# Performance work log

Measured on AMD Instinct MI355X. Metric: run time of the kernel, lower is better.

## Reference

```python
import jax, jax.numpy as jnp
import numpy as np

ALPHA = 0.5
BETA = 5.0
LOGIT_SCALE = 100.0  # exp(log(100)) -- CLIP's learned logit scale at its clamp value
NUM_CLASSES = 200


def _l2norm(x):
    return x / jnp.linalg.norm(x, axis=-1, keepdims=True)


def setup_inputs() -> dict:
    key = jax.random.key(0)
    k1, k2, k3, k4 = jax.random.split(key, 4)
    img_f = jax.random.normal(k1, (1024, 512), dtype=jnp.float32)
    text_features = jax.random.normal(k2, (200, 512), dtype=jnp.float32)
    keys = jax.random.normal(k3, (50000, 512), dtype=jnp.float32)
    labels = jax.random.randint(k4, (50000,), 0, NUM_CLASSES, dtype=jnp.int64)
    return {"img_f": img_f, "text_features": text_features, "keys": keys, "labels": labels}


def reference(img_f, text_features, keys, labels):
    # encode_image output is L2-normalized in the module; keys were built from
    # normalized image features, text_features are normalized class embeddings.
    q = _l2norm(img_f)            # [B, D]
    t = _l2norm(text_features)    # [C, D]
    k = _l2norm(keys)             # [N, D]

    # CLIP zero-shot branch: scale * q @ t.T -> [B, C]
    z = LOGIT_SCALE * jnp.einsum('bd,cd->bc', q, t)

    # Tip-Adapter cache branch: exp(beta * q @ keys.T) @ one_hot(labels)
    sim = jnp.einsum('bd,nd->bn', q, k)                 # [B, N]
    aff = jnp.exp(BETA * sim)                           # [B, N]
    values = jax.nn.one_hot(labels, NUM_CLASSES, dtype=aff.dtype)  # [N, C]
    c = aff @ values                                    # [B, C]

    return (1.0 - ALPHA) * z + ALPHA * c
```

## Files before the change

### kernel.cpp

```cpp
#include <hip/hip_runtime.h>

#define B_Q    1024
#define D_K    512
#define N_CLS  200
#define N_KEYS 50000
#define N_PAD  50176
#define N_ZT   196
#define NT_TOT 197
#define KN_ROWS 50200
#define HS     16

#define PR0 N_KEYS
#define PR1 (PR0 + B_Q)
#define PR2 (PR1 + N_CLS)
#define PR3 (PR2 + 400)

typedef __attribute__((ext_vector_type(8))) short bf16x8;
typedef __attribute__((ext_vector_type(4))) float f32x4;

__device__ __forceinline__ unsigned short f2bf(float f) {
  union { float f; unsigned int i; } v; v.f = f;
  unsigned int r = v.i + 0x7fffu + ((v.i >> 16) & 1u);
  return (unsigned short)(r >> 16);
}
__device__ __forceinline__ uint4 pack8(const float f[8], float s) {
  uint4 o;
  o.x = (unsigned)f2bf(f[0]*s) | ((unsigned)f2bf(f[1]*s) << 16);
  o.y = (unsigned)f2bf(f[2]*s) | ((unsigned)f2bf(f[3]*s) << 16);
  o.z = (unsigned)f2bf(f[4]*s) | ((unsigned)f2bf(f[5]*s) << 16);
  o.w = (unsigned)f2bf(f[6]*s) | ((unsigned)f2bf(f[7]*s) << 16);
  return o;
}
__device__ __forceinline__ void async_copy16(const void* g, void* lds) {
  __builtin_amdgcn_global_load_lds(
      (const __attribute__((address_space(1))) unsigned int*)g,
      (__attribute__((address_space(3))) unsigned int*)lds, 16, 0, 0);
}

__global__ void k_zero(int* __restrict__ g) {
  int i = blockIdx.x * 1024 + threadIdx.x;
  if (i < 2 * N_CLS * HS) g[i] = 0;
}

__global__ __launch_bounds__(1024) void k_rank(const int* __restrict__ labels,
                                               const int* __restrict__ ghist,
                                               int* __restrict__ gcnt,
                                               int* __restrict__ perm,
                                               int* __restrict__ cls) {
  __shared__ int incl[N_CLS];
  __shared__ int histl[N_CLS];
  __shared__ int lhist[N_CLS];
  __shared__ int lbase[N_CLS];
  __shared__ int lcur[N_CLS];
  int t = threadIdx.x;
  if (t < N_CLS) {
    int h = ghist[t * HS];
    histl[t] = h; incl[t] = h; lhist[t] = 0;
  }
  __syncthreads();
  for (int d = 1; d < N_CLS; d <<= 1) {
    int x = 0;
    if (t < N_CLS && t >= d) x = incl[t - d];
    __syncthreads();
    if (t < N_CLS) incl[t] += x;
    __syncthreads();
  }
  int n = blockIdx.x * 1024 + t;
  int lab = -1;
  if (n < N_KEYS) {
    lab = labels[n];
    atomicAdd(&lhist[lab], 1);
  }
  __syncthreads();
  if (t < N_CLS && lhist[t] > 0) {
    lbase[t] = (incl[t] - histl[t]) + atomicAdd(&gcnt[t * HS], lhist[t]);
    lcur[t] = 0;
  }
  __syncthreads();
  if (n < N_KEYS) {
    int r = atomicAdd(&lcur[lab], 1);
    int d = lbase[lab] + r;
    perm[d] = n;
    cls[d] = lab;
  } else if (n < N_PAD) {
    perm[n] = N_KEYS;
    cls[n] = N_CLS;
  }
}

__global__ void k_prep2(const float* __restrict__ keys, const float* __restrict__ img,
                        const float* __restrict__ txt, const int* __restrict__ labels,
                        unsigned short* __restrict__ qn, unsigned short* __restrict__ kn,
                        int* __restrict__ ghist, float* __restrict__ out) {
  int w = threadIdx.x >> 6, lane = threadIdx.x & 63;
  int row = blockIdx.x * 4 + w;
  const float* src; unsigned short* dst;
  if (row < PR0) {
    if (lane == 0) atomicAdd(&ghist[labels[row] * HS], 1);
    src = keys + (size_t)row * D_K;
    dst = kn + (size_t)row * D_K;
  } else if (row < PR1) {
    int r = row - PR0;
    src = img + (size_t)r * D_K;
    dst = qn + (size_t)r * D_K;
  } else if (row < PR2) {
    int r = row - PR1;
    src = txt + (size_t)r * D_K;
    dst = kn + (size_t)(N_KEYS + r) * D_K;
  } else if (row < PR3) {
    int zr = row - PR2;
    uint4* o4 = (uint4*)(out + (size_t)zr * 512) + lane * 2;
    o4[0] = make_uint4(0, 0, 0, 0);
    o4[1] = make_uint4(0, 0, 0, 0);
    return;
  } else return;
  const float4* s4 = (const float4*)src + lane * 2;
  float4 a = s4[0], b = s4[1];
  float f[8] = {a.x, a.y, a.z, a.w, b.x, b.y, b.z, b.w};
  float ss = 0.f;
#pragma unroll
  for (int i = 0; i < 8; i++) ss += f[i] * f[i];
#pragma unroll
  for (int d = 1; d < 64; d <<= 1) ss += __shfl_xor(ss, d);
  float rinv = rsqrtf(ss);
  *((uint4*)dst + lane) = pack8(f, rinv);
}

__global__ __launch_bounds__(512, 2) void k_main(const unsigned short* __restrict__ qn,
                                                 const unsigned short* __restrict__ kn,
                                                 const int* __restrict__ cls,
                                                 const int* __restrict__ perm,
                                                 float* __restrict__ out) {
  extern __shared__ unsigned short smem[];
  int t = threadIdx.x;
  int bid = blockIdx.x;
  int xcd = bid & 7, bk = bid >> 3;
  int wsw = (xcd < 4 ? xcd * 99 : 396 + (xcd - 4) * 98) + bk;
  int tileN = wsw >> 2, tileB = wsw & 3;
  int rowB0 = tileB * 256, rowN0 = tileN * 256;

  f32x4 acc[8][4];
#pragma unroll
  for (int i = 0; i < 8; i++)
#pragma unroll
    for (int j = 0; j < 4; j++) acc[i][j] = (f32x4){0.f, 0.f, 0.f, 0.f};

  int lane = t & 63, w = t >> 6;
  int wm = (w >> 2) * 128;
  int wcN = (w & 3) * 64;
  int l15 = lane & 15, lq = lane >> 4;
  const int rA = t >> 3;
  const int gsw = ((t & 7) ^ (rA & 7)) * 8;
  const int sw = l15 & 7;

  int prow[4];
  int cj[4] = {N_CLS, N_CLS, N_CLS, N_CLS};
  int cseg0 = N_CLS, cseg1 = N_CLS;
  if (tileN < N_ZT) {
#pragma unroll
    for (int c = 0; c < 4; c++) prow[c] = perm[rowN0 + c * 64 + rA];
#pragma unroll
    for (int j = 0; j < 4; j++) cj[j] = cls[rowN0 + wcN + 16 * j + l15];
    cseg0 = cls[rowN0 + wcN];
    cseg1 = cls[rowN0 + wcN + 63];
  } else {
#pragma unroll
    for (int c = 0; c < 4; c++) {
      int r = c * 64 + rA;
      prow[c] = N_KEYS + (r < N_CLS ? r : N_CLS - 1);
    }
  }

  auto stageA = [&](int p, int k0) {
    unsigned short* dst = smem + p * 16384;
#pragma unroll
    for (int c = 0; c < 4; c++)
      async_copy16(qn + (size_t)(rowB0 + c * 64 + rA) * D_K + k0 + gsw,
                   dst + c * 4096 + t * 8);
  };
  auto stageB = [&](int p, int k0) {
    unsigned short* dst = smem + 32768 + p * 16384;
#pragma unroll
    for (int c = 0; c < 4; c++)
      async_copy16(kn + (size_t)prow[c] * D_K + k0 + gsw,
                   dst + c * 4096 + t * 8);
  };
  auto quad = [&](int p, int ih, int jh) {
    const unsigned short* A = smem + p * 16384;
    const unsigned short* B = smem + 32768 + p * 16384;
    __builtin_amdgcn_s_setprio(1);
#pragma unroll
    for (int s = 0; s < 2; s++) {
      int cg = ((s * 4 + lq) ^ sw) * 8;
      bf16x8 af[4], bf[2];
#pragma unroll
      for (int i = 0; i < 4; i++) {
        int ra = wm + ih * 64 + 16 * i + l15;
        af[i] = *(const bf16x8*)&A[ra * 64 + cg];
      }
#pragma unroll
      for (int jj = 0; jj < 2; jj++) {
        int rb = wcN + (jh * 2 + jj) * 16 + l15;
        bf[jj] = *(const bf16x8*)&B[rb * 64 + cg];
      }
#pragma unroll
      for (int i = 0; i < 4; i++)
#pragma unroll
        for (int jj = 0; jj < 2; jj++)
          acc[ih * 4 + i][jh * 2 + jj] = __builtin_amdgcn_mfma_f32_16x16x32_bf16(
              af[i], bf[jj], acc[ih * 4 + i][jh * 2 + jj], 0, 0, 0);
    }
    __builtin_amdgcn_s_setprio(0);
  };

  stageA(0, 0); stageB(0, 0);
  __syncthreads();
  for (int kt = 0; kt < 8; ++kt) {
    int p = kt & 1, k0n = (kt + 1) * 64;
    if (kt < 7) stageA(p ^ 1, k0n);
    quad(p, 0, 0);
    __builtin_amdgcn_s_barrier();
    if (kt < 7) stageB(p ^ 1, k0n);
    quad(p, 0, 1);
    __builtin_amdgcn_s_barrier();
    quad(p, 1, 0);
    __builtin_amdgcn_s_barrier();
    quad(p, 1, 1);
    __syncthreads();
  }

  if (tileN >= N_ZT) {
#pragma unroll
    for (int i = 0; i < 8; i++)
#pragma unroll
      for (int j = 0; j < 4; j++) {
        int col = wcN + 16 * j + l15;
        if (col < N_CLS) {
#pragma unroll
          for (int r = 0; r < 4; r++) {
            int row = rowB0 + wm + 16 * i + lq * 4 + r;
            atomicAdd(out + (size_t)row * N_CLS + col, 50.0f * acc[i][j][r]);
          }
        }
      }
    return;
  }

#pragma unroll
  for (int i = 0; i < 8; i++)
#pragma unroll
    for (int j = 0; j < 4; j++)
#pragma unroll
      for (int r = 0; r < 4; r++) acc[i][j][r] = __expf(5.0f * acc[i][j][r]);

  for (int c = cseg0; c <= cseg1; c++) {
    if (c >= N_CLS) break;
#pragma unroll
    for (int i = 0; i < 8; i++) {
      float s0 = 0.f, s1 = 0.f, s2 = 0.f, s3 = 0.f;
#pragma unroll
      for (int j = 0; j < 4; j++) {
        if (cj[j] == c) {
          s0 += acc[i][j][0]; s1 += acc[i][j][1];
          s2 += acc[i][j][2]; s3 += acc[i][j][3];
        }
      }
#pragma unroll
      for (int d = 1; d < 16; d <<= 1) {
        s0 += __shfl_xor(s0, d); s1 += __shfl_xor(s1, d);
        s2 += __shfl_xor(s2, d); s3 += __shfl_xor(s3, d);
      }
      if (l15 == 0) {
        int row = rowB0 + wm + 16 * i + lq * 4;
        float* o = out + (size_t)row * N_CLS + c;
        if (s0 != 0.f) atomicAdd(o + 0 * N_CLS, 0.5f * s0);
        if (s1 != 0.f) atomicAdd(o + 1 * N_CLS, 0.5f * s1);
        if (s2 != 0.f) atomicAdd(o + 2 * N_CLS, 0.5f * s2);
        if (s3 != 0.f) atomicAdd(o + 3 * N_CLS, 0.5f * s3);
      }
    }
  }
}

extern "C" void kernel_launch(void* const* d_in, const int* in_sizes, int n_in,
                              void* d_out, int out_size, void* d_ws, size_t ws_size,
                              hipStream_t stream) {
  (void)in_sizes; (void)n_in; (void)out_size; (void)ws_size;
  const float* img    = (const float*)d_in[0];
  const float* txt    = (const float*)d_in[1];
  const float* keys   = (const float*)d_in[2];
  const int*   labels = (const int*)d_in[3];
  float*       out    = (float*)d_out;

  char* ws = (char*)d_ws;
  unsigned short* qn = (unsigned short*)(ws + 0);
  unsigned short* kn = (unsigned short*)(ws + 1048576);
  int*  perm = (int*)(ws + 52453376);
  int*  cls  = (int*)(ws + 52654080);
  int*  gz   = (int*)(ws + 52854784);

  hipFuncSetAttribute((const void*)k_main,
                      hipFuncAttributeMaxDynamicSharedMemorySize, 131072);

  k_zero<<<7, 1024, 0, stream>>>(gz);
  k_prep2<<<(PR3 + 3) / 4, 256, 0, stream>>>(keys, img, txt, labels, qn, kn, gz, out);
  k_rank<<<N_PAD / 1024, 1024, 0, stream>>>(labels, gz, gz + N_CLS * HS, perm, cls);
  k_main<<<dim3(4 * NT_TOT), 512, 131072, stream>>>(qn, kn, cls, perm, out);
}
```

Before: 290.1 us.

## Halve B-tile to 128 rows, doubling grid and cutting LDS and accumulators

Shrinks each block's query tile from 256 to 128 rows, so the grid doubles to 8x197 blocks, per-wave accumulators halve, and dynamic LDS drops from 128KB to 96KB. The A fragments are loaded once per k-substep and reused across both B column halves. The block-to-XCD mapping is also simplified. The aim is more blocks in flight and lower register pressure, at the cost of loading the key tiles twice as often and issuing more atomics for the class reduction.

```diff
diff --git a/kernel.cpp b/kernel.cpp
--- a/kernel.cpp
+++ b/kernel.cpp
@@ -134,20 +134,19 @@
   extern __shared__ unsigned short smem[];
   int t = threadIdx.x;
   int bid = blockIdx.x;
-  int xcd = bid & 7, bk = bid >> 3;
-  int wsw = (xcd < 4 ? xcd * 99 : 396 + (xcd - 4) * 98) + bk;
-  int tileN = wsw >> 2, tileB = wsw & 3;
-  int rowB0 = tileB * 256, rowN0 = tileN * 256;
-
-  f32x4 acc[8][4];
-#pragma unroll
-  for (int i = 0; i < 8; i++)
+  int wsw = (bid & 7) * NT_TOT + (bid >> 3);
+  int tileN = wsw >> 3, tileB = wsw & 7;
+  int rowB0 = tileB * 128, rowN0 = tileN * 256;
+
+  f32x4 acc[4][4];
+#pragma unroll
+  for (int i = 0; i < 4; i++)
 #pragma unroll
     for (int j = 0; j < 4; j++) acc[i][j] = (f32x4){0.f, 0.f, 0.f, 0.f};
 
   int lane = t & 63, w = t >> 6;
-  int wm = (w >> 2) * 128;
-  int wcN = (w & 3) * 64;
+  int wr = (w >> 2) * 64;
+  int wc = (w & 3) * 64;
   int l15 = lane & 15, lq = lane >> 4;
   const int rA = t >> 3;
   const int gsw = ((t & 7) ^ (rA & 7)) * 8;
@@ -160,9 +159,9 @@
 #pragma unroll
     for (int c = 0; c < 4; c++) prow[c] = perm[rowN0 + c * 64 + rA];
 #pragma unroll
-    for (int j = 0; j < 4; j++) cj[j] = cls[rowN0 + wcN + 16 * j + l15];
-    cseg0 = cls[rowN0 + wcN];
-    cseg1 = cls[rowN0 + wcN + 63];
+    for (int j = 0; j < 4; j++) cj[j] = cls[rowN0 + wc + 16 * j + l15];
+    cseg0 = cls[rowN0 + wc];
+    cseg1 = cls[rowN0 + wc + 63];
   } else {
 #pragma unroll
     for (int c = 0; c < 4; c++) {
@@ -172,44 +171,46 @@
   }
 
   auto stageA = [&](int p, int k0) {
-    unsigned short* dst = smem + p * 16384;
-#pragma unroll
-    for (int c = 0; c < 4; c++)
+    unsigned short* dst = smem + p * 8192;
+#pragma unroll
+    for (int c = 0; c < 2; c++)
       async_copy16(qn + (size_t)(rowB0 + c * 64 + rA) * D_K + k0 + gsw,
                    dst + c * 4096 + t * 8);
   };
   auto stageB = [&](int p, int k0) {
-    unsigned short* dst = smem + 32768 + p * 16384;
+    unsigned short* dst = smem + 16384 + p * 16384;
 #pragma unroll
     for (int c = 0; c < 4; c++)
       async_copy16(kn + (size_t)prow[c] * D_K + k0 + gsw,
                    dst + c * 4096 + t * 8);
   };
-  auto quad = [&](int p, int ih, int jh) {
-    const unsigned short* A = smem + p * 16384;
-    const unsigned short* B = smem + 32768 + p * 16384;
+
+  bf16x8 af[4];
+  auto ldA = [&](int p, int s) {
+    const unsigned short* A = smem + p * 8192;
+    int cg = ((s * 4 + lq) ^ sw) * 8;
+#pragma unroll
+    for (int i = 0; i < 4; i++) {
+      int ra = wr + 16 * i + l15;
+      af[i] = *(const bf16x8*)&A[ra * 64 + cg];
+    }
+  };
+  auto mfma8 = [&](int p, int s, int jh) {
+    const unsigned short* B = smem + 16384 + p * 16384;
+    int cg = ((s * 4 + lq) ^ sw) * 8;
+    bf16x8 bf[2];
+#pragma unroll
+    for (int jj = 0; jj < 2; jj++) {
+      int rb = wc + (jh * 2 + jj) * 16 + l15;
+      bf[jj] = *(const bf16x8*)&B[rb * 64 + cg];
+    }
     __builtin_amdgcn_s_setprio(1);
 #pragma unroll
-    for (int s = 0; s < 2; s++) {
-      int cg = ((s * 4 + lq) ^ sw) * 8;
-      bf16x8 af[4], bf[2];
-#pragma unroll
-      for (int i = 0; i < 4; i++) {
-        int ra = wm + ih * 64 + 16 * i + l15;
-        af[i] = *(const bf16x8*)&A[ra * 64 + cg];
-      }
-#pragma unroll
-      for (int jj = 0; jj < 2; jj++) {
-        int rb = wcN + (jh * 2 + jj) * 16 + l15;
-        bf[jj] = *(const bf16x8*)&B[rb * 64 + cg];
-      }
-#pragma unroll
-      for (int i = 0; i < 4; i++)
-#pragma unroll
-        for (int jj = 0; jj < 2; jj++)
-          acc[ih * 4 + i][jh * 2 + jj] = __builtin_amdgcn_mfma_f32_16x16x32_bf16(
-              af[i], bf[jj], acc[ih * 4 + i][jh * 2 + jj], 0, 0, 0);
-    }
+    for (int i = 0; i < 4; i++)
+#pragma unroll
+      for (int jj = 0; jj < 2; jj++)
+        acc[i][jh * 2 + jj] = __builtin_amdgcn_mfma_f32_16x16x32_bf16(
+            af[i], bf[jj], acc[i][jh * 2 + jj], 0, 0, 0);
     __builtin_amdgcn_s_setprio(0);
   };
 
@@ -218,27 +219,29 @@
   for (int kt = 0; kt < 8; ++kt) {
     int p = kt & 1, k0n = (kt + 1) * 64;
     if (kt < 7) stageA(p ^ 1, k0n);
-    quad(p, 0, 0);
+    ldA(p, 0);
+    mfma8(p, 0, 0);
     __builtin_amdgcn_s_barrier();
     if (kt < 7) stageB(p ^ 1, k0n);
-    quad(p, 0, 1);
+    mfma8(p, 0, 1);
     __builtin_amdgcn_s_barrier();
-    quad(p, 1, 0);
+    ldA(p, 1);
+    mfma8(p, 1, 0);
     __builtin_amdgcn_s_barrier();
-    quad(p, 1, 1);
+    mfma8(p, 1, 1);
     __syncthreads();
   }
 
   if (tileN >= N_ZT) {
 #pragma unroll
-    for (int i = 0; i < 8; i++)
+    for (int i = 0; i < 4; i++)
 #pragma unroll
       for (int j = 0; j < 4; j++) {
-        int col = wcN + 16 * j + l15;
+        int col = wc + 16 * j + l15;
         if (col < N_CLS) {
 #pragma unroll
           for (int r = 0; r < 4; r++) {
-            int row = rowB0 + wm + 16 * i + lq * 4 + r;
+            int row = rowB0 + wr + 16 * i + lq * 4 + r;
             atomicAdd(out + (size_t)row * N_CLS + col, 50.0f * acc[i][j][r]);
           }
         }
@@ -247,7 +250,7 @@
   }
 
 #pragma unroll
-  for (int i = 0; i < 8; i++)
+  for (int i = 0; i < 4; i++)
 #pragma unroll
     for (int j = 0; j < 4; j++)
 #pragma unroll
@@ -256,7 +259,7 @@
   for (int c = cseg0; c <= cseg1; c++) {
     if (c >= N_CLS) break;
 #pragma unroll
-    for (int i = 0; i < 8; i++) {
+    for (int i = 0; i < 4; i++) {
       float s0 = 0.f, s1 = 0.f, s2 = 0.f, s3 = 0.f;
 #pragma unroll
       for (int j = 0; j < 4; j++) {
@@ -271,7 +274,7 @@
         s2 += __shfl_xor(s2, d); s3 += __shfl_xor(s3, d);
       }
       if (l15 == 0) {
-        int row = rowB0 + wm + 16 * i + lq * 4;
+        int row = rowB0 + wr + 16 * i + lq * 4;
         float* o = out + (size_t)row * N_CLS + c;
         if (s0 != 0.f) atomicAdd(o + 0 * N_CLS, 0.5f * s0);
         if (s1 != 0.f) atomicAdd(o + 1 * N_CLS, 0.5f * s1);
@@ -300,10 +303,10 @@
   int*  gz   = (int*)(ws + 52854784);
 
   hipFuncSetAttribute((const void*)k_main,
-                      hipFuncAttributeMaxDynamicSharedMemorySize, 131072);
+                      hipFuncAttributeMaxDynamicSharedMemorySize, 98304);
 
   k_zero<<<7, 1024, 0, stream>>>(gz);
   k_prep2<<<(PR3 + 3) / 4, 256, 0, stream>>>(keys, img, txt, labels, qn, kn, gz, out);
   k_rank<<<N_PAD / 1024, 1024, 0, stream>>>(labels, gz, gz + N_CLS * HS, perm, cls);
-  k_main<<<dim3(4 * NT_TOT), 512, 131072, stream>>>(qn, kn, cls, perm, out);
-}
+  k_main<<<dim3(8 * NT_TOT), 512, 98304, stream>>>(qn, kn, cls, perm, out);
+}
```

Measured after the change: 274.1 us. 5.5% less time.
